# Kernel optimization log

Measured on AMD Instinct MI355X. Metric: run time of the kernel, lower is better.

## Reference

```python
import jax, jax.numpy as jnp
import numpy as np

N = 20000
E = 320000
IN_DIM, HID, MID, OUT, HEADS = 1536, 512, 128, 5, 8
NEG_SLOPE = 0.2
BN_EPS = 1e-5


def gat_conv(x, edge_index, W, a_src, a_dst, bias, heads, out_ch):
    """PyG-style GATConv (eval mode, self-loops already in edge_index).
    x: [N, F_in]; W: [F_in, heads*out_ch]; a_src/a_dst: [heads, out_ch]; bias: [heads*out_ch].
    Returns [N, heads*out_ch] (head concat)."""
    n = x.shape[0]
    h = (x @ W).reshape(n, heads, out_ch)              # [N,H,C]
    src, dst = edge_index[0], edge_index[1]
    al_s = jnp.sum(h * a_src, axis=-1)                 # [N,H]
    al_d = jnp.sum(h * a_dst, axis=-1)                 # [N,H]
    e = al_s[src] + al_d[dst]                          # [E,H]
    e = jnp.where(e >= 0, e, NEG_SLOPE * e)            # leaky_relu
    # segment softmax over incoming edges per dst node
    e_max = jax.ops.segment_max(e, dst, num_segments=n)
    e_max = jnp.where(jnp.isfinite(e_max), e_max, 0.0)
    ex = jnp.exp(e - e_max[dst])                       # [E,H]
    denom = jax.ops.segment_sum(ex, dst, num_segments=n)
    alpha = ex / (denom[dst] + 1e-16)                  # [E,H]
    msg = h[src] * alpha[:, :, None]                   # [E,H,C]
    out = jax.ops.segment_sum(msg, dst, num_segments=n)
    return out.reshape(n, heads * out_ch) + bias


def bn_eval(x, gamma, beta, mean, var):
    return (x - mean) * jax.lax.rsqrt(var + BN_EPS) * gamma + beta


def setup_inputs() -> dict:
    key = jax.random.key(0)
    ks = jax.random.split(key, 24)
    x = jax.random.normal(ks[0], (N, IN_DIM), dtype=jnp.float32)
    edge_index = jax.random.randint(ks[1], (2, E), 0, N, dtype=jnp.int32)

    def glorot(k, shape):
        fan = shape[0] + shape[-1]
        return jax.random.normal(k, shape, dtype=jnp.float32) * np.sqrt(2.0 / fan)

    inp = {"x": x, "edge_index": edge_index}
    # conv1: 1536 -> 8 heads x 64
    inp["W1"] = glorot(ks[2], (IN_DIM, HID))
    inp["as1"] = glorot(ks[3], (HEADS, HID // HEADS))
    inp["ad1"] = glorot(ks[4], (HEADS, HID // HEADS))
    inp["b1"] = jnp.zeros((HID,), jnp.float32)
    # conv2: 512 -> 8 heads x 16
    inp["W2"] = glorot(ks[5], (HID, MID))
    inp["as2"] = glorot(ks[6], (HEADS, MID // HEADS))
    inp["ad2"] = glorot(ks[7], (HEADS, MID // HEADS))
    inp["b2"] = jnp.zeros((MID,), jnp.float32)
    # conv3: 128 -> 1 head x 5
    inp["W3"] = glorot(ks[8], (MID, OUT))
    inp["as3"] = glorot(ks[9], (1, OUT))
    inp["ad3"] = glorot(ks[10], (1, OUT))
    inp["b3"] = jnp.zeros((OUT,), jnp.float32)
    # batchnorm params (eval mode, running stats)
    inp["g1"] = jax.random.normal(ks[11], (HID,), jnp.float32) * 0.1 + 1.0
    inp["be1"] = jax.random.normal(ks[12], (HID,), jnp.float32) * 0.1
    inp["m1"] = jax.random.normal(ks[13], (HID,), jnp.float32) * 0.1
    inp["v1"] = jax.random.uniform(ks[14], (HID,), jnp.float32, 0.5, 1.5)
    inp["g2"] = jax.random.normal(ks[15], (MID,), jnp.float32) * 0.1 + 1.0
    inp["be2"] = jax.random.normal(ks[16], (MID,), jnp.float32) * 0.1
    inp["m2"] = jax.random.normal(ks[17], (MID,), jnp.float32) * 0.1
    inp["v2"] = jax.random.uniform(ks[18], (MID,), jnp.float32, 0.5, 1.5)
    return inp


def reference(x, edge_index, W1, as1, ad1, b1, W2, as2, ad2, b2, W3, as3, ad3, b3,
              g1, be1, m1, v1, g2, be2, m2, v2):
    # add self-loops (PyG GATConv default)
    loops = jnp.arange(N, dtype=edge_index.dtype)
    ei = jnp.concatenate([edge_index, jnp.stack([loops, loops])], axis=1)

    h = jax.nn.relu(gat_conv(x, ei, W1, as1, ad1, b1, HEADS, HID // HEADS))
    h = bn_eval(h, g1, be1, m1, v1)
    h = jax.nn.relu(gat_conv(h, ei, W2, as2, ad2, b2, HEADS, MID // HEADS))
    h = bn_eval(h, g2, be2, m2, v2)
    h = gat_conv(h, ei, W3, as3, ad3, b3, 1, OUT)
    return jax.nn.log_softmax(h, axis=1)
```

## Files before the change

### kernel.cpp

```cpp
#include <hip/hip_runtime.h>
#include <math.h>

#define IN_DIM 1536
#define HID 512
#define MID 128
#define OUTC 5
#define HEADS 8
#define NEG_SLOPE 0.2f
#define BN_EPS 1e-5f

typedef __attribute__((ext_vector_type(8))) short s16x8;
typedef __attribute__((ext_vector_type(4))) float fx4;

__device__ __forceinline__ unsigned short bf16_rne(float f) {
    unsigned int u = __float_as_uint(f);
    u += 0x7fffu + ((u >> 16) & 1u);
    return (unsigned short)(u >> 16);
}
__device__ __forceinline__ float bf16_to_f32(unsigned short u) {
    return __uint_as_float((unsigned int)u << 16);
}

__device__ __forceinline__ void async_copy16(void* lds, const void* g) {
    __builtin_amdgcn_global_load_lds(
        (const __attribute__((address_space(1))) unsigned int*)g,
        (__attribute__((address_space(3))) unsigned int*)lds, 16, 0, 0);
}

__global__ void hist_kernel(const int* __restrict__ ei, int* __restrict__ deg,
                            int ET, int E) {
    int e = blockIdx.x * blockDim.x + threadIdx.x;
    if (e >= ET) return;
    int dst = (e < E) ? ei[E + e] : (e - E);
    atomicAdd(&deg[dst], 1);
}

__global__ __launch_bounds__(1024) void scan_kernel(const int* __restrict__ deg,
                                                    int* __restrict__ row_ptr,
                                                    int* __restrict__ cursor, int n) {
    __shared__ int partial[1024];
    int tid = threadIdx.x;
    int per = (n + 1023) / 1024;
    int base = tid * per;
    int s = 0;
    for (int i = 0; i < per; ++i) {
        int idx = base + i;
        if (idx < n) s += deg[idx];
    }
    partial[tid] = s;
    __syncthreads();
    for (int off = 1; off < 1024; off <<= 1) {
        int v = (tid >= off) ? partial[tid - off] : 0;
        __syncthreads();
        partial[tid] += v;
        __syncthreads();
    }
    int prefix = (tid == 0) ? 0 : partial[tid - 1];
    for (int i = 0; i < per; ++i) {
        int idx = base + i;
        if (idx < n) {
            row_ptr[idx] = prefix;
            cursor[idx] = prefix;
            prefix += deg[idx];
        }
    }
    if (tid == 1023) row_ptr[n] = partial[1023];
}

__global__ void scatter_kernel(const int* __restrict__ ei, int* __restrict__ cursor,
                               int* __restrict__ csr_src, int ET, int E) {
    int e = blockIdx.x * blockDim.x + threadIdx.x;
    if (e >= ET) return;
    int src, dst;
    if (e < E) { src = ei[e]; dst = ei[E + e]; }
    else       { src = dst = e - E; }
    int slot = atomicAdd(&cursor[dst], 1);
    csr_src[slot] = src;
}

__global__ void cvt_bf16_kernel(const float* __restrict__ in,
                                unsigned short* __restrict__ out, int n4) {
    int i = blockIdx.x * blockDim.x + threadIdx.x;
    if (i >= n4) return;
    float4 v = ((const float4*)in)[i];
    ushort4 o;
    o.x = bf16_rne(v.x); o.y = bf16_rne(v.y);
    o.z = bf16_rne(v.z); o.w = bf16_rne(v.w);
    ((ushort4*)out)[i] = o;
}

__global__ __launch_bounds__(256) void transpose_both_kernel(
    const float* __restrict__ W1, unsigned short* __restrict__ W1h,
    const float* __restrict__ W2, unsigned short* __restrict__ W2h,
    unsigned short* __restrict__ W2l) {
    __shared__ float tile[32][33];
    int b = blockIdx.x;
    const float* W;
    unsigned short *Th, *Tl;
    int K, Nn, kb, nb;
    bool wlo;
    if (b < 768) {
        W = W1; Th = W1h; Tl = nullptr; wlo = false; K = IN_DIM; Nn = HID;
        nb = (b & 15) * 32; kb = (b >> 4) * 32;
    } else {
        int b2 = b - 768;
        W = W2; Th = W2h; Tl = W2l; wlo = true; K = HID; Nn = MID;
        nb = (b2 & 3) * 32; kb = (b2 >> 2) * 32;
    }
    int tx = threadIdx.x & 31, ty = threadIdx.x >> 5;
#pragma unroll
    for (int r = 0; r < 4; ++r)
        tile[ty + r * 8][tx] = W[(size_t)(kb + ty + r * 8) * Nn + nb + tx];
    __syncthreads();
#pragma unroll
    for (int r = 0; r < 4; ++r) {
        int n = ty + r * 8;
        float v = tile[tx][n];
        unsigned short hi = bf16_rne(v);
        size_t o = (size_t)(nb + n) * K + kb + tx;
        Th[o] = hi;
        if (wlo) {
            float hif = __uint_as_float((unsigned int)hi << 16);
            Tl[o] = bf16_rne(v - hif);
        }
    }
}

__global__ __launch_bounds__(256) void gemm1_kernel(
    const unsigned short* __restrict__ A, const unsigned short* __restrict__ Bh,
    unsigned short* __restrict__ Cb, const float* __restrict__ a_s,
    const float* __restrict__ a_d, float* __restrict__ als,
    float* __restrict__ ald, int M, int N, int K, int MBLK) {
    int b = blockIdx.x;
    int xm = (b & 7) + 8 * (b >> 5);
    int ym = (b >> 3) & 3;
    if (xm >= MBLK) return;

    __shared__ unsigned short Asb[2][128 * 32];
    __shared__ unsigned short Bsb[2][128 * 32];

    const int tid = threadIdx.x;
    const int lane = tid & 63;
    const int wv = tid >> 6;
    const int row0 = xm * 128;
    const int nb0 = ym * 128;
    const int col = lane & 15;
    const int quad = lane >> 4;
    const int m0 = (wv >> 1) * 64;
    const int n0 = (wv & 1) * 64;

    const int s_row = lane >> 2;
    const int s_chunk = (lane & 3) ^ ((lane >> 3) & 3);
    int agr0 = row0 + (wv * 2 + 0) * 16 + s_row; if (agr0 >= M) agr0 = M - 1;
    int agr1 = row0 + (wv * 2 + 1) * 16 + s_row; if (agr1 >= M) agr1 = M - 1;
    const size_t ag0 = (size_t)agr0 * K + s_chunk * 8;
    const size_t ag1 = (size_t)agr1 * K + s_chunk * 8;
    const size_t bg0 = (size_t)(nb0 + (wv * 2 + 0) * 16 + s_row) * K + s_chunk * 8;
    const size_t bg1 = (size_t)(nb0 + (wv * 2 + 1) * 16 + s_row) * K + s_chunk * 8;

    const int rsw = (col >> 1) & 3;

    fx4 acc[4][4];
#pragma unroll
    for (int i = 0; i < 4; ++i)
#pragma unroll
        for (int j = 0; j < 4; ++j) acc[i][j] = (fx4){0.f, 0.f, 0.f, 0.f};

    async_copy16(&Asb[0][(wv * 2 + 0) * 512], A + ag0);
    async_copy16(&Asb[0][(wv * 2 + 1) * 512], A + ag1);
    async_copy16(&Bsb[0][(wv * 2 + 0) * 512], Bh + bg0);
    async_copy16(&Bsb[0][(wv * 2 + 1) * 512], Bh + bg1);
    __syncthreads();

    int cur = 0;
    for (int k0 = 0; k0 < K; k0 += 32) {
        const int nxt = cur ^ 1;
        if (k0 + 32 < K) {
            const int kn = k0 + 32;
            async_copy16(&Asb[nxt][(wv * 2 + 0) * 512], A + ag0 + kn);
            async_copy16(&Asb[nxt][(wv * 2 + 1) * 512], A + ag1 + kn);
            async_copy16(&Bsb[nxt][(wv * 2 + 0) * 512], Bh + bg0 + kn);
            async_copy16(&Bsb[nxt][(wv * 2 + 1) * 512], Bh + bg1 + kn);
        }
        s16x8 afr[4], bfr[4];
#pragma unroll
        for (int i = 0; i < 4; ++i)
            afr[i] = *(const s16x8*)&Asb[cur][(m0 + i * 16 + col) * 32 + (quad ^ rsw) * 8];
#pragma unroll
        for (int j = 0; j < 4; ++j)
            bfr[j] = *(const s16x8*)&Bsb[cur][(n0 + j * 16 + col) * 32 + (quad ^ rsw) * 8];
#pragma unroll
        for (int i = 0; i < 4; ++i)
#pragma unroll
            for (int j = 0; j < 4; ++j)
                acc[i][j] = __builtin_amdgcn_mfma_f32_16x16x32_bf16(afr[i], bfr[j], acc[i][j], 0, 0, 0);
        __syncthreads();
        cur = nxt;
    }

#pragma unroll
    for (int i = 0; i < 4; ++i) {
        int gr0 = row0 + m0 + i * 16 + quad * 4;
#pragma unroll
        for (int j = 0; j < 4; ++j) {
            int gc = nb0 + n0 + j * 16 + col;
#pragma unroll
            for (int r = 0; r < 4; ++r) {
                int gr = gr0 + r;
                if (gr < M) Cb[(size_t)gr * N + gc] = bf16_rne(acc[i][j][r]);
            }
        }
    }

    const int head = (nb0 + n0) >> 6;
    float asv[4], adv[4];
#pragma unroll
    for (int j = 0; j < 4; ++j) {
        asv[j] = a_s[head * 64 + j * 16 + col];
        adv[j] = a_d[head * 64 + j * 16 + col];
    }
#pragma unroll
    for (int i = 0; i < 4; ++i) {
#pragma unroll
        for (int r = 0; r < 4; ++r) {
            float ss = acc[i][0][r] * asv[0] + acc[i][1][r] * asv[1] +
                       acc[i][2][r] * asv[2] + acc[i][3][r] * asv[3];
            float sd = acc[i][0][r] * adv[0] + acc[i][1][r] * adv[1] +
                       acc[i][2][r] * adv[2] + acc[i][3][r] * adv[3];
#pragma unroll
            for (int off = 8; off; off >>= 1) {
                ss += __shfl_xor(ss, off);
                sd += __shfl_xor(sd, off);
            }
            if (col == 0) {
                int gr = row0 + m0 + i * 16 + quad * 4 + r;
                if (gr < M) {
                    als[gr * HEADS + head] = ss;
                    ald[gr * HEADS + head] = sd;
                }
            }
        }
    }
}

__global__ __launch_bounds__(256) void gemm2_kernel(
    const unsigned short* __restrict__ A, const unsigned short* __restrict__ Bh,
    const unsigned short* __restrict__ Bl, unsigned short* __restrict__ Cb,
    const float* __restrict__ a_s, const float* __restrict__ a_d,
    float* __restrict__ als, float* __restrict__ ald, int M, int N, int K) {
    __shared__ unsigned short Asb[2][32 * 32];
    __shared__ unsigned short Bhb[2][128 * 32];
    __shared__ unsigned short Blb[2][128 * 32];

    const int tid = threadIdx.x;
    const int lane = tid & 63;
    const int wv = tid >> 6;
    const int row0 = blockIdx.x * 32;
    const int col = lane & 15;
    const int quad = lane >> 4;
    const int m0 = (wv >> 1) * 16;
    const int n0 = (wv & 1) * 64;
    const int b_row = lane >> 2;
    const int b_chunk = (lane & 3) ^ ((lane >> 3) & 3);
    const int rsw = (col >> 1) & 3;

    const int t0 = wv * 2, t1 = t0 + 1;
    const size_t bgo0 = (size_t)(t0 * 16 + b_row) * K + b_chunk * 8;
    const size_t bgo1 = (size_t)(t1 * 16 + b_row) * K + b_chunk * 8;
    int agr = row0 + wv * 16 + b_row; if (agr >= M) agr = M - 1;
    const size_t ago = (size_t)agr * K + b_chunk * 8;

    fx4 acc[4];
#pragma unroll
    for (int j = 0; j < 4; ++j) acc[j] = (fx4){0.f, 0.f, 0.f, 0.f};

    auto stage = [&](int buf, int k) {
        async_copy16(&Bhb[buf][t0 * 512], Bh + bgo0 + k);
        async_copy16(&Bhb[buf][t1 * 512], Bh + bgo1 + k);
        async_copy16(&Blb[buf][t0 * 512], Bl + bgo0 + k);
        async_copy16(&Blb[buf][t1 * 512], Bl + bgo1 + k);
        if (wv < 2) async_copy16(&Asb[buf][wv * 512], A + ago + k);
    };

    stage(0, 0);
    __syncthreads();

    int cur = 0;
    for (int k0 = 0; k0 < K; k0 += 32) {
        const int nxt = cur ^ 1;
        if (k0 + 32 < K) stage(nxt, k0 + 32);
        s16x8 a, bh4[4], bl4[4];
        a = *(const s16x8*)&Asb[cur][(m0 + col) * 32 + (quad ^ rsw) * 8];
#pragma unroll
        for (int j = 0; j < 4; ++j) {
            int rb = (n0 + j * 16 + col) * 32 + (quad ^ rsw) * 8;
            bh4[j] = *(const s16x8*)&Bhb[cur][rb];
            bl4[j] = *(const s16x8*)&Blb[cur][rb];
        }
#pragma unroll
        for (int j = 0; j < 4; ++j) {
            acc[j] = __builtin_amdgcn_mfma_f32_16x16x32_bf16(a, bl4[j], acc[j], 0, 0, 0);
            acc[j] = __builtin_amdgcn_mfma_f32_16x16x32_bf16(a, bh4[j], acc[j], 0, 0, 0);
        }
        __syncthreads();
        cur = nxt;
    }

    int gr0 = row0 + m0 + quad * 4;
#pragma unroll
    for (int j = 0; j < 4; ++j) {
        int gc = n0 + j * 16 + col;
#pragma unroll
        for (int r = 0; r < 4; ++r) {
            int gr = gr0 + r;
            if (gr < M) Cb[(size_t)gr * N + gc] = bf16_rne(acc[j][r]);
        }
    }

    float asv[4], adv[4];
#pragma unroll
    for (int j = 0; j < 4; ++j) {
        asv[j] = a_s[n0 + j * 16 + col];
        adv[j] = a_d[n0 + j * 16 + col];
    }
#pragma unroll
    for (int j = 0; j < 4; ++j) {
        int head = (n0 >> 4) + j;
#pragma unroll
        for (int r = 0; r < 4; ++r) {
            float ss = acc[j][r] * asv[j];
            float sd = acc[j][r] * adv[j];
#pragma unroll
            for (int off = 8; off; off >>= 1) {
                ss += __shfl_xor(ss, off);
                sd += __shfl_xor(sd, off);
            }
            if (col == 0) {
                int gr = gr0 + r;
                if (gr < M) {
                    als[gr * HEADS + head] = ss;
                    ald[gr * HEADS + head] = sd;
                }
            }
        }
    }
}

__global__ __launch_bounds__(256) void agg1_wave_kernel(
    const unsigned short* __restrict__ hlin, const float* __restrict__ als,
    const float* __restrict__ ald, const int* __restrict__ row_ptr,
    const int* __restrict__ csr_src, const float* __restrict__ bias,
    const float* __restrict__ gamma, const float* __restrict__ beta,
    const float* __restrict__ mean, const float* __restrict__ var,
    unsigned short* __restrict__ outh, int n) {
    int lane = threadIdx.x & 63;
    int dst = blockIdx.x * 4 + (threadIdx.x >> 6);
    if (dst >= n) return;
    const int f0 = lane * 8;
    const int h = lane >> 3;
    const int j8 = lane >> 3;
    const int ch = lane & 7;
    float ald_c = ald[dst * HEADS + ch];

    int s0 = row_ptr[dst], s1 = row_ptr[dst + 1];
    float acc[8];
#pragma unroll
    for (int v = 0; v < 8; ++v) acc[v] = 0.f;
    float den = 0.f;

    for (int base = s0; base < s1; base += 8) {
        int take = min(8, s1 - base);
        float ex = 0.f;
        int src_l = 0;
        if (j8 < take) {
            src_l = csr_src[base + j8];
            float e = als[src_l * HEADS + ch] + ald_c;
            e = (e >= 0.f) ? e : NEG_SLOPE * e;
            ex = __expf(e);
        }
        for (int jj = 0; jj < take; ++jj) {
            int src = __shfl(src_l, jj * 8);
            float a = __shfl(ex, jj * 8 + h);
            den += a;
            union { s16x8 v; unsigned short u[8]; } w;
            w.v = *(const s16x8*)&hlin[(size_t)src * HID + f0];
#pragma unroll
            for (int v = 0; v < 8; ++v) acc[v] += a * bf16_to_f32(w.u[v]);
        }
    }

    float rd = 1.f / (den + 1e-16f);
    union { s16x8 v; unsigned short u[8]; } o;
#pragma unroll
    for (int v = 0; v < 8; ++v) {
        int f = f0 + v;
        float val = acc[v] * rd + bias[f];
        val = fmaxf(val, 0.f);
        val = (val - mean[f]) * rsqrtf(var[f] + BN_EPS) * gamma[f] + beta[f];
        o.u[v] = bf16_rne(val);
    }
    *(s16x8*)&outh[(size_t)dst * HID + f0] = o.v;
}

__global__ __launch_bounds__(128) void agg2_l3_kernel(
    const unsigned short* __restrict__ hlin, const float* __restrict__ als,
    const float* __restrict__ ald, const int* __restrict__ row_ptr,
    const int* __restrict__ csr_src, const float* __restrict__ bias,
    const float* __restrict__ gamma, const float* __restrict__ beta,
    const float* __restrict__ mean, const float* __restrict__ var,
    const float* __restrict__ W3, const float* __restrict__ as3,
    const float* __restrict__ ad3, float* __restrict__ h3lin,
    float* __restrict__ als3, float* __restrict__ ald3) {
    int dst = blockIdx.x;
    int tid = threadIdx.x;
    int h = tid >> 4;
    __shared__ float exs[16][8];
    __shared__ int srcs[16];
    __shared__ float red[2][OUTC];
    int s0 = row_ptr[dst], s1 = row_ptr[dst + 1];
    int cj = tid >> 3, ch = tid & 7;
    float ald_c = ald[dst * HEADS + ch];
    float acc = 0.f, den = 0.f;

    for (int base = s0; base < s1; base += 16) {
        int take = min(16, s1 - base);
        if (cj < take) {
            int src = csr_src[base + cj];
            if (ch == 0) srcs[cj] = src;
            float e = als[src * HEADS + ch] + ald_c;
            e = (e >= 0.f) ? e : NEG_SLOPE * e;
            exs[cj][ch] = __expf(e);
        }
        __syncthreads();
        for (int jj = 0; jj < take; ++jj) {
            int src = srcs[jj];
            float a = exs[jj][h];
            den += a;
            acc += a * bf16_to_f32(hlin[(size_t)src * MID + tid]);
        }
        __syncthreads();
    }

    float val = acc / (den + 1e-16f) + bias[tid];
    val = fmaxf(val, 0.f);
    val = (val - mean[tid]) * rsqrtf(var[tid] + BN_EPS) * gamma[tid] + beta[tid];

    float p[OUTC];
#pragma unroll
    for (int c = 0; c < OUTC; ++c) p[c] = val * W3[tid * OUTC + c];
#pragma unroll
    for (int off = 32; off; off >>= 1) {
#pragma unroll
        for (int c = 0; c < OUTC; ++c) p[c] += __shfl_xor(p[c], off);
    }
    int wv = tid >> 6;
    if ((tid & 63) == 0) {
#pragma unroll
        for (int c = 0; c < OUTC; ++c) red[wv][c] = p[c];
    }
    __syncthreads();
    if (tid == 0) {
        float ss = 0.f, sd = 0.f;
#pragma unroll
        for (int c = 0; c < OUTC; ++c) {
            float v = red[0][c] + red[1][c];
            h3lin[(size_t)dst * OUTC + c] = v;
            ss += v * as3[c];
            sd += v * ad3[c];
        }
        als3[dst] = ss;
        ald3[dst] = sd;
    }
}

__global__ __launch_bounds__(256) void agg3_lsm_kernel(
    const float* __restrict__ h3lin, const float* __restrict__ als,
    const float* __restrict__ ald, const int* __restrict__ row_ptr,
    const int* __restrict__ csr_src, const float* __restrict__ b3,
    float* __restrict__ out, int n) {
    int g = blockIdx.x * blockDim.x + threadIdx.x;
    int dst = g >> 4;
    int l = g & 15;
    if (dst >= n) return;
    int s0 = row_ptr[dst], s1 = row_ptr[dst + 1];
    float ad = ald[dst];
    float den = 0.f;
    float acc[OUTC] = {0.f, 0.f, 0.f, 0.f, 0.f};
    for (int j = s0 + l; j < s1; j += 16) {
        int src = csr_src[j];
        float e = als[src] + ad;
        e = (e >= 0.f) ? e : NEG_SLOPE * e;
        float x = __expf(e);
        den += x;
        const float* hp = h3lin + (size_t)src * OUTC;
#pragma unroll
        for (int c = 0; c < OUTC; ++c) acc[c] += x * hp[c];
    }
#pragma unroll
    for (int off = 8; off; off >>= 1) {
        den += __shfl_xor(den, off);
#pragma unroll
        for (int c = 0; c < OUTC; ++c) acc[c] += __shfl_xor(acc[c], off);
    }
    if (l == 0) {
        float rd = 1.f / (den + 1e-16f);
        float m = -INFINITY;
#pragma unroll
        for (int c = 0; c < OUTC; ++c) {
            acc[c] = acc[c] * rd + b3[c];
            m = fmaxf(m, acc[c]);
        }
        float s = 0.f;
#pragma unroll
        for (int c = 0; c < OUTC; ++c) s += __expf(acc[c] - m);
        float lse = m + __logf(s);
#pragma unroll
        for (int c = 0; c < OUTC; ++c) out[(size_t)dst * OUTC + c] = acc[c] - lse;
    }
}

extern "C" void kernel_launch(void* const* d_in, const int* in_sizes, int n_in,
                              void* d_out, int out_size, void* d_ws, size_t ws_size,
                              hipStream_t stream) {
    const float* x   = (const float*)d_in[0];
    const int*   ei  = (const int*)d_in[1];
    const float* W1  = (const float*)d_in[2];
    const float* as1 = (const float*)d_in[3];
    const float* ad1 = (const float*)d_in[4];
    const float* b1  = (const float*)d_in[5];
    const float* W2  = (const float*)d_in[6];
    const float* as2 = (const float*)d_in[7];
    const float* ad2 = (const float*)d_in[8];
    const float* b2  = (const float*)d_in[9];
    const float* W3  = (const float*)d_in[10];
    const float* as3 = (const float*)d_in[11];
    const float* ad3 = (const float*)d_in[12];
    const float* b3  = (const float*)d_in[13];
    const float* g1  = (const float*)d_in[14];
    const float* be1 = (const float*)d_in[15];
    const float* m1  = (const float*)d_in[16];
    const float* v1  = (const float*)d_in[17];
    const float* g2  = (const float*)d_in[18];
    const float* be2 = (const float*)d_in[19];
    const float* m2  = (const float*)d_in[20];
    const float* v2  = (const float*)d_in[21];

    const int N = in_sizes[0] / IN_DIM;
    const int E = in_sizes[1] / 2;
    const int ET = E + N;
    const int MBLK1 = (N + 127) / 128;
    const int MBLK2 = (N + 31) / 32;

    char* ws = (char*)d_ws;
    size_t off = 0;
    auto take = [&](size_t bytes) -> char* {
        char* p = ws + off;
        off += (bytes + 255) & ~(size_t)255;
        return p;
    };
    int* deg      = (int*)take((size_t)N * 4);
    int* row_ptr  = (int*)take((size_t)(N + 1) * 4);
    int* cursor   = (int*)take((size_t)N * 4);
    int* csr_src  = (int*)take((size_t)ET * 4);
    unsigned short* W1h = (unsigned short*)take((size_t)HID * IN_DIM * 2);
    unsigned short* W2h = (unsigned short*)take((size_t)MID * HID * 2);
    unsigned short* W2l = (unsigned short*)take((size_t)MID * HID * 2);
    unsigned short* xh  = (unsigned short*)take((size_t)N * IN_DIM * 2);
    unsigned short* h1lin = (unsigned short*)take((size_t)N * HID * 2);
    unsigned short* h1h   = (unsigned short*)take((size_t)N * HID * 2);
    unsigned short* h2lin = (unsigned short*)take((size_t)N * MID * 2);
    float* h3lin  = (float*)take((size_t)N * OUTC * 4);
    float* als    = (float*)take((size_t)N * HEADS * 4);
    float* ald    = (float*)take((size_t)N * HEADS * 4);
    float* als3   = (float*)take((size_t)N * 4);
    float* ald3   = (float*)take((size_t)N * 4);

    hipMemsetAsync(deg, 0, (size_t)N * 4, stream);
    hist_kernel<<<(ET + 255) / 256, 256, 0, stream>>>(ei, deg, ET, E);
    scan_kernel<<<1, 1024, 0, stream>>>(deg, row_ptr, cursor, N);
    scatter_kernel<<<(ET + 255) / 256, 256, 0, stream>>>(ei, cursor, csr_src, ET, E);
    transpose_both_kernel<<<832, 256, 0, stream>>>(W1, W1h, W2, W2h, W2l);
    {
        int n4 = N * IN_DIM / 4;
        cvt_bf16_kernel<<<(n4 + 255) / 256, 256, 0, stream>>>(x, xh, n4);
    }

    gemm1_kernel<<<640, 256, 0, stream>>>(xh, W1h, h1lin, as1, ad1, als, ald,
                                          N, HID, IN_DIM, MBLK1);
    agg1_wave_kernel<<<(N + 3) / 4, 256, 0, stream>>>(
        h1lin, als, ald, row_ptr, csr_src, b1, g1, be1, m1, v1, h1h, N);

    gemm2_kernel<<<MBLK2, 256, 0, stream>>>(h1h, W2h, W2l, h2lin, as2, ad2,
                                            als, ald, N, MID, HID);
    agg2_l3_kernel<<<N, 128, 0, stream>>>(
        h2lin, als, ald, row_ptr, csr_src, b2, g2, be2, m2, v2,
        W3, as3, ad3, h3lin, als3, ald3);

    agg3_lsm_kernel<<<(N * 16 + 255) / 256, 256, 0, stream>>>(
        h3lin, als3, ald3, row_ptr, csr_src, b3, (float*)d_out, N);
}
```

Baseline: 446.7 us.

## Fuse prep kernels, batch row loads in agg1, make agg2 wave-per-node

Replaces the memset, weight transpose and x-to-bf16 conversion with a single prep kernel that dispatches on block index, cutting launch count. In agg1 the gathered neighbor rows for each 8-edge chunk are all loaded up front before accumulation, so several gather loads are in flight at once. agg2_l3 becomes one wave per destination node with two features per lane and no shared memory or block barriers, where before it used a 128-thread block per node. The fused prep kernel changes ordering: degree zeroing now happens in the same launch as the conversions, and the prefetched rows raise register pressure.

```diff
diff --git a/kernel.cpp b/kernel.cpp
--- a/kernel.cpp
+++ b/kernel.cpp
@@ -78,52 +78,60 @@
     csr_src[slot] = src;
 }
 
-__global__ void cvt_bf16_kernel(const float* __restrict__ in,
-                                unsigned short* __restrict__ out, int n4) {
-    int i = blockIdx.x * blockDim.x + threadIdx.x;
+#define ZB 20
+__global__ __launch_bounds__(256) void prep_kernel(
+    int* __restrict__ deg, int n_deg4,
+    const float* __restrict__ W1, unsigned short* __restrict__ W1h,
+    const float* __restrict__ W2, unsigned short* __restrict__ W2h,
+    unsigned short* __restrict__ W2l,
+    const float* __restrict__ x, unsigned short* __restrict__ xh, int n4) {
+    int b = blockIdx.x;
+    if (b < ZB) {
+        int i = b * 256 + threadIdx.x;
+        if (i < n_deg4) ((int4*)deg)[i] = make_int4(0, 0, 0, 0);
+        return;
+    }
+    if (b < ZB + 832) {
+        __shared__ float tile[32][33];
+        int tb = b - ZB;
+        const float* W;
+        unsigned short *Th, *Tl;
+        int K, Nn, kb, nb;
+        bool wlo;
+        if (tb < 768) {
+            W = W1; Th = W1h; Tl = nullptr; wlo = false; K = IN_DIM; Nn = HID;
+            nb = (tb & 15) * 32; kb = (tb >> 4) * 32;
+        } else {
+            int b2 = tb - 768;
+            W = W2; Th = W2h; Tl = W2l; wlo = true; K = HID; Nn = MID;
+            nb = (b2 & 3) * 32; kb = (b2 >> 2) * 32;
+        }
+        int tx = threadIdx.x & 31, ty = threadIdx.x >> 5;
+#pragma unroll
+        for (int r = 0; r < 4; ++r)
+            tile[ty + r * 8][tx] = W[(size_t)(kb + ty + r * 8) * Nn + nb + tx];
+        __syncthreads();
+#pragma unroll
+        for (int r = 0; r < 4; ++r) {
+            int n = ty + r * 8;
+            float v = tile[tx][n];
+            unsigned short hi = bf16_rne(v);
+            size_t o = (size_t)(nb + n) * K + kb + tx;
+            Th[o] = hi;
+            if (wlo) {
+                float hif = __uint_as_float((unsigned int)hi << 16);
+                Tl[o] = bf16_rne(v - hif);
+            }
+        }
+        return;
+    }
+    int i = (b - ZB - 832) * 256 + threadIdx.x;
     if (i >= n4) return;
-    float4 v = ((const float4*)in)[i];
+    float4 v = ((const float4*)x)[i];
     ushort4 o;
     o.x = bf16_rne(v.x); o.y = bf16_rne(v.y);
     o.z = bf16_rne(v.z); o.w = bf16_rne(v.w);
-    ((ushort4*)out)[i] = o;
-}
-
-__global__ __launch_bounds__(256) void transpose_both_kernel(
-    const float* __restrict__ W1, unsigned short* __restrict__ W1h,
-    const float* __restrict__ W2, unsigned short* __restrict__ W2h,
-    unsigned short* __restrict__ W2l) {
-    __shared__ float tile[32][33];
-    int b = blockIdx.x;
-    const float* W;
-    unsigned short *Th, *Tl;
-    int K, Nn, kb, nb;
-    bool wlo;
-    if (b < 768) {
-        W = W1; Th = W1h; Tl = nullptr; wlo = false; K = IN_DIM; Nn = HID;
-        nb = (b & 15) * 32; kb = (b >> 4) * 32;
-    } else {
-        int b2 = b - 768;
-        W = W2; Th = W2h; Tl = W2l; wlo = true; K = HID; Nn = MID;
-        nb = (b2 & 3) * 32; kb = (b2 >> 2) * 32;
-    }
-    int tx = threadIdx.x & 31, ty = threadIdx.x >> 5;
-#pragma unroll
-    for (int r = 0; r < 4; ++r)
-        tile[ty + r * 8][tx] = W[(size_t)(kb + ty + r * 8) * Nn + nb + tx];
-    __syncthreads();
-#pragma unroll
-    for (int r = 0; r < 4; ++r) {
-        int n = ty + r * 8;
-        float v = tile[tx][n];
-        unsigned short hi = bf16_rne(v);
-        size_t o = (size_t)(nb + n) * K + kb + tx;
-        Th[o] = hi;
-        if (wlo) {
-            float hif = __uint_as_float((unsigned int)hi << 16);
-            Tl[o] = bf16_rne(v - hif);
-        }
-    }
+    ((ushort4*)xh)[i] = o;
 }
 
 __global__ __launch_bounds__(256) void gemm1_kernel(
@@ -378,14 +386,24 @@
             e = (e >= 0.f) ? e : NEG_SLOPE * e;
             ex = __expf(e);
         }
-        for (int jj = 0; jj < take; ++jj) {
-            int src = __shfl(src_l, jj * 8);
-            float a = __shfl(ex, jj * 8 + h);
-            den += a;
-            union { s16x8 v; unsigned short u[8]; } w;
-            w.v = *(const s16x8*)&hlin[(size_t)src * HID + f0];
-#pragma unroll
-            for (int v = 0; v < 8; ++v) acc[v] += a * bf16_to_f32(w.u[v]);
+        s16x8 rows[8];
+#pragma unroll
+        for (int jj = 0; jj < 8; ++jj) {
+            if (jj < take) {
+                int src = __shfl(src_l, jj * 8);
+                rows[jj] = *(const s16x8*)&hlin[(size_t)src * HID + f0];
+            }
+        }
+#pragma unroll
+        for (int jj = 0; jj < 8; ++jj) {
+            if (jj < take) {
+                float a = __shfl(ex, jj * 8 + h);
+                den += a;
+                union { s16x8 v; unsigned short u[8]; } w;
+                w.v = rows[jj];
+#pragma unroll
+                for (int v = 0; v < 8; ++v) acc[v] += a * bf16_to_f32(w.u[v]);
+            }
         }
     }
 
@@ -402,7 +420,7 @@
     *(s16x8*)&outh[(size_t)dst * HID + f0] = o.v;
 }
 
-__global__ __launch_bounds__(128) void agg2_l3_kernel(
+__global__ __launch_bounds__(256) void agg2_l3_wave_kernel(
     const unsigned short* __restrict__ hlin, const float* __restrict__ als,
     const float* __restrict__ ald, const int* __restrict__ row_ptr,
     const int* __restrict__ csr_src, const float* __restrict__ bias,
@@ -410,63 +428,72 @@
     const float* __restrict__ mean, const float* __restrict__ var,
     const float* __restrict__ W3, const float* __restrict__ as3,
     const float* __restrict__ ad3, float* __restrict__ h3lin,
-    float* __restrict__ als3, float* __restrict__ ald3) {
-    int dst = blockIdx.x;
-    int tid = threadIdx.x;
-    int h = tid >> 4;
-    __shared__ float exs[16][8];
-    __shared__ int srcs[16];
-    __shared__ float red[2][OUTC];
+    float* __restrict__ als3, float* __restrict__ ald3, int n) {
+    int lane = threadIdx.x & 63;
+    int dst = blockIdx.x * 4 + (threadIdx.x >> 6);
+    if (dst >= n) return;
+    const int f0 = lane * 2;
+    const int h = lane >> 3;
+    const int j8 = lane >> 3;
+    const int ch = lane & 7;
+    float ald_c = ald[dst * HEADS + ch];
+
     int s0 = row_ptr[dst], s1 = row_ptr[dst + 1];
-    int cj = tid >> 3, ch = tid & 7;
-    float ald_c = ald[dst * HEADS + ch];
-    float acc = 0.f, den = 0.f;
-
-    for (int base = s0; base < s1; base += 16) {
-        int take = min(16, s1 - base);
-        if (cj < take) {
-            int src = csr_src[base + cj];
-            if (ch == 0) srcs[cj] = src;
-            float e = als[src * HEADS + ch] + ald_c;
+    float acc0 = 0.f, acc1 = 0.f, den = 0.f;
+
+    for (int base = s0; base < s1; base += 8) {
+        int take = min(8, s1 - base);
+        float ex = 0.f;
+        int src_l = 0;
+        if (j8 < take) {
+            src_l = csr_src[base + j8];
+            float e = als[src_l * HEADS + ch] + ald_c;
             e = (e >= 0.f) ? e : NEG_SLOPE * e;
-            exs[cj][ch] = __expf(e);
-        }
-        __syncthreads();
-        for (int jj = 0; jj < take; ++jj) {
-            int src = srcs[jj];
-            float a = exs[jj][h];
-            den += a;
-            acc += a * bf16_to_f32(hlin[(size_t)src * MID + tid]);
-        }
-        __syncthreads();
-    }
-
-    float val = acc / (den + 1e-16f) + bias[tid];
-    val = fmaxf(val, 0.f);
-    val = (val - mean[tid]) * rsqrtf(var[tid] + BN_EPS) * gamma[tid] + beta[tid];
+            ex = __expf(e);
+        }
+        unsigned int rows[8];
+#pragma unroll
+        for (int jj = 0; jj < 8; ++jj) {
+            if (jj < take) {
+                int src = __shfl(src_l, jj * 8);
+                rows[jj] = *(const unsigned int*)&hlin[(size_t)src * MID + f0];
+            }
+        }
+#pragma unroll
+        for (int jj = 0; jj < 8; ++jj) {
+            if (jj < take) {
+                float a = __shfl(ex, jj * 8 + h);
+                den += a;
+                acc0 += a * bf16_to_f32((unsigned short)(rows[jj] & 0xffffu));
+                acc1 += a * bf16_to_f32((unsigned short)(rows[jj] >> 16));
+            }
+        }
+    }
+
+    float rd = 1.f / (den + 1e-16f);
+    float val0 = acc0 * rd + bias[f0];
+    val0 = fmaxf(val0, 0.f);
+    val0 = (val0 - mean[f0]) * rsqrtf(var[f0] + BN_EPS) * gamma[f0] + beta[f0];
+    float val1 = acc1 * rd + bias[f0 + 1];
+    val1 = fmaxf(val1, 0.f);
+    val1 = (val1 - mean[f0 + 1]) * rsqrtf(var[f0 + 1] + BN_EPS) * gamma[f0 + 1] + beta[f0 + 1];
 
     float p[OUTC];
 #pragma unroll
-    for (int c = 0; c < OUTC; ++c) p[c] = val * W3[tid * OUTC + c];
+    for (int c = 0; c < OUTC; ++c)
+        p[c] = val0 * W3[f0 * OUTC + c] + val1 * W3[(f0 + 1) * OUTC + c];
 #pragma unroll
     for (int off = 32; off; off >>= 1) {
 #pragma unroll
         for (int c = 0; c < OUTC; ++c) p[c] += __shfl_xor(p[c], off);
     }
-    int wv = tid >> 6;
-    if ((tid & 63) == 0) {
-#pragma unroll
-        for (int c = 0; c < OUTC; ++c) red[wv][c] = p[c];
-    }
-    __syncthreads();
-    if (tid == 0) {
+    if (lane == 0) {
         float ss = 0.f, sd = 0.f;
 #pragma unroll
         for (int c = 0; c < OUTC; ++c) {
-            float v = red[0][c] + red[1][c];
-            h3lin[(size_t)dst * OUTC + c] = v;
-            ss += v * as3[c];
-            sd += v * ad3[c];
+            h3lin[(size_t)dst * OUTC + c] = p[c];
+            ss += p[c] * as3[c];
+            sd += p[c] * ad3[c];
         }
         als3[dst] = ss;
         ald3[dst] = sd;
@@ -575,15 +602,15 @@
     float* als3   = (float*)take((size_t)N * 4);
     float* ald3   = (float*)take((size_t)N * 4);
 
-    hipMemsetAsync(deg, 0, (size_t)N * 4, stream);
+    {
+        int n4 = N * IN_DIM / 4;
+        int nb_cvt = (n4 + 255) / 256;
+        prep_kernel<<<ZB + 832 + nb_cvt, 256, 0, stream>>>(
+            deg, N / 4, W1, W1h, W2, W2h, W2l, x, xh, n4);
+    }
     hist_kernel<<<(ET + 255) / 256, 256, 0, stream>>>(ei, deg, ET, E);
     scan_kernel<<<1, 1024, 0, stream>>>(deg, row_ptr, cursor, N);
     scatter_kernel<<<(ET + 255) / 256, 256, 0, stream>>>(ei, cursor, csr_src, ET, E);
-    transpose_both_kernel<<<832, 256, 0, stream>>>(W1, W1h, W2, W2h, W2l);
-    {
-        int n4 = N * IN_DIM / 4;
-        cvt_bf16_kernel<<<(n4 + 255) / 256, 256, 0, stream>>>(x, xh, n4);
-    }
 
     gemm1_kernel<<<640, 256, 0, stream>>>(xh, W1h, h1lin, as1, ad1, als, ald,
                                           N, HID, IN_DIM, MBLK1);
@@ -592,9 +619,9 @@
 
     gemm2_kernel<<<MBLK2, 256, 0, stream>>>(h1h, W2h, W2l, h2lin, as2, ad2,
                                             als, ald, N, MID, HID);
-    agg2_l3_kernel<<<N, 128, 0, stream>>>(
+    agg2_l3_wave_kernel<<<(N + 3) / 4, 256, 0, stream>>>(
         h2lin, als, ald, row_ptr, csr_src, b2, g2, be2, m2, v2,
-        W3, as3, ad3, h3lin, als3, ald3);
+        W3, as3, ad3, h3lin, als3, ald3, N);
 
     agg3_lsm_kernel<<<(N * 16 + 255) / 256, 256, 0, stream>>>(
         h3lin, als3, ald3, row_ptr, csr_src, b3, (float*)d_out, N);
```

Measured after the change: 444.8 us. No clear change (-0.4%).
